# Optimization experiments

Hardware: AMD Instinct MI355X
Metric: run time of the kernel (lower is better)

The kernel has to match this reference:

```python
import jax, jax.numpy as jnp
import numpy as np

D_MODEL = 256
NUM_HEADS = 8
HEAD_DIM = D_MODEL // NUM_HEADS


def setup_inputs() -> dict:
    key = jax.random.key(0)
    ks = jax.random.split(key, 16)
    B, C, H, W = 2, D_MODEL, 64, 64
    s = 0.02
    inp = {
        "query_feat": jax.random.normal(ks[0], (B, C, H, W), jnp.float32),
        "lateral_feat": jax.random.normal(ks[1], (B, C, H, W), jnp.float32),
        # 1x1 convs == per-pixel linear layers: weight (out, in), bias (out,)
        "Wq": jax.random.normal(ks[2], (C, C), jnp.float32) * s,
        "bq": jnp.zeros((C,), jnp.float32),
        "Wk": jax.random.normal(ks[3], (C, C), jnp.float32) * s,
        "bk": jnp.zeros((C,), jnp.float32),
        "Wv": jax.random.normal(ks[4], (C, C), jnp.float32) * s,
        "bv": jnp.zeros((C,), jnp.float32),
        "Wo": jax.random.normal(ks[5], (C, C), jnp.float32) * s,
        "bo": jnp.zeros((C,), jnp.float32),
        "W1": jax.random.normal(ks[6], (4 * C, C), jnp.float32) * s,
        "b1": jnp.zeros((4 * C,), jnp.float32),
        "W2": jax.random.normal(ks[7], (C, 4 * C), jnp.float32) * s,
        "b2": jnp.zeros((C,), jnp.float32),
    }
    return inp


def reference(query_feat, lateral_feat, Wq, bq, Wk, bk, Wv, bv, Wo, bo, W1, b1, W2, b2):
    B, C, H, W = query_feat.shape
    N = H * W
    h, d = NUM_HEADS, HEAD_DIM
    scale = d ** -0.5

    # (B,C,H,W) -> (B,N,C) tokens
    xq = query_feat.reshape(B, C, N).transpose(0, 2, 1)
    xl = lateral_feat.reshape(B, C, N).transpose(0, 2, 1)

    # 1x1-conv projections = dense per-token linear
    Q = (xq @ Wq.T + bq).reshape(B, N, h, d).transpose(0, 2, 1, 3)  # (B,h,N,d)
    K = (xl @ Wk.T + bk).reshape(B, N, h, d).transpose(0, 2, 1, 3)
    V = (xl @ Wv.T + bv).reshape(B, N, h, d).transpose(0, 2, 1, 3)

    scores = jnp.einsum("bhqd,bhkd->bhqk", Q, K) * scale  # (B,h,N,N)
    attn = jax.nn.softmax(scores, axis=-1)  # dropout = identity at inference
    out = jnp.einsum("bhqk,bhkd->bhqd", attn, V)  # (B,h,N,d)

    out = out.transpose(0, 2, 1, 3).reshape(B, N, C)  # (B,N,C)
    out = out @ Wo.T + bo
    out = out.transpose(0, 2, 1).reshape(B, C, H, W)
    out = out + query_feat  # residual

    # MLP on channels (1x1 convs + exact GELU)
    t = out.reshape(B, C, N).transpose(0, 2, 1)  # (B,N,C)
    hdn = jax.nn.gelu(t @ W1.T + b1, approximate=False)  # (B,N,4C)
    mlp = (hdn @ W2.T + b2).transpose(0, 2, 1).reshape(B, C, H, W)
    return out + mlp
```

## Files before the change

kernel.cpp:

```cpp
#include <hip/hip_runtime.h>
#include <math.h>

namespace {

constexpr int kB  = 2;
constexpr int kC  = 256;
constexpr int kN  = 4096;
constexpr int kHD = 32;
constexpr int kC4 = 1024;

typedef __attribute__((ext_vector_type(8))) short bf16x8;
typedef __attribute__((ext_vector_type(4))) float f32x4;
typedef __attribute__((ext_vector_type(16))) float f32x16;

__device__ __forceinline__ float gelu_exact(float x) {
  return 0.5f * x * (1.0f + erff(x * 0.70710678118654752f));
}

__device__ __forceinline__ unsigned short f2bf(float x) {
  unsigned u = __builtin_bit_cast(unsigned, x);
  u += 0x7FFFu + ((u >> 16) & 1u);
  return (unsigned short)(u >> 16);
}

__device__ __forceinline__ float bf2f(unsigned short us) {
  return __builtin_bit_cast(float, (unsigned)us << 16);
}

__device__ __forceinline__ float fast_exp2(float x) {
  int i = (int)__builtin_fmaf(x, 8388608.0f, 1064866805.0f);
  return __builtin_bit_cast(float, i);
}

__device__ __forceinline__ unsigned cvt_pk_bf16(float lo, float hi) {
  unsigned r;
  asm("v_cvt_pk_bf16_f32 %0, %1, %2" : "=v"(r) : "v"(lo), "v"(hi));
  return r;
}

__global__ __launch_bounds__(256)
void convert_all(const float* __restrict__ qfeat, const float* __restrict__ lfeat,
                 const float* __restrict__ Wq, const float* __restrict__ Wk,
                 const float* __restrict__ Wv, const float* __restrict__ Wo,
                 const float* __restrict__ W1, const float* __restrict__ W2,
                 unsigned short* __restrict__ qtok, unsigned short* __restrict__ ltok,
                 unsigned short* __restrict__ wbf)
{
  __shared__ float Lds[32][36];
  const int z = blockIdx.z;
  const int t = threadIdx.x;
  if (z < 4) {
    const float* src = (z < kB) ? qfeat : lfeat;
    unsigned short* dst = (z < kB) ? qtok : ltok;
    const int b = z & 1;
    src += (size_t)b * kC * kN;
    dst += (size_t)b * kN * kC;
    const int n0 = blockIdx.x * 32, c0 = blockIdx.y * 32;
    const int r = t >> 3, q4 = (t & 7) * 4;
    {
      const float4 v = *(const float4*)&src[(size_t)(c0 + r) * kN + n0 + q4];
      Lds[r][q4 + 0] = v.x; Lds[r][q4 + 1] = v.y; Lds[r][q4 + 2] = v.z; Lds[r][q4 + 3] = v.w;
    }
    __syncthreads();
    ushort4 p;
    p.x = f2bf(Lds[q4 + 0][r]); p.y = f2bf(Lds[q4 + 1][r]);
    p.z = f2bf(Lds[q4 + 2][r]); p.w = f2bf(Lds[q4 + 3][r]);
    *(ushort4*)&dst[(size_t)(n0 + r) * kC + c0 + q4] = p;
  } else {
    const int wi = blockIdx.y * 128 + blockIdx.x;
    if (wi >= 768) return;
    const int i4 = wi * 1024 + t * 4;
    const float* s; int base;
    if      (i4 < 65536)  { s = Wq; base = 0; }
    else if (i4 < 131072) { s = Wk; base = 65536; }
    else if (i4 < 196608) { s = Wv; base = 131072; }
    else if (i4 < 262144) { s = Wo; base = 196608; }
    else if (i4 < 524288) { s = W1; base = 262144; }
    else                  { s = W2; base = 524288; }
    const float4 v = *(const float4*)&s[i4 - base];
    ushort4 p;
    p.x = f2bf(v.x); p.y = f2bf(v.y); p.z = f2bf(v.z); p.w = f2bf(v.w);
    *(ushort4*)&wbf[i4] = p;
  }
}

template <int EPI, bool GELU, bool RES>
__global__ __launch_bounds__(256)
void gemm_mfma(const unsigned short* __restrict__ Wbf,
               const unsigned short* __restrict__ Xtok,
               const float* __restrict__ bias, const float* __restrict__ res,
               void* __restrict__ Y1, void* __restrict__ Y2,
               int M, int Nn, int K, float oscale)
{
  __shared__ unsigned short Wlds[64 * 64];
  __shared__ unsigned short Xlds[64 * 64];

  const int z = blockIdx.z;
  Xtok += (size_t)z * Nn * K;

  const int t = threadIdx.x;
  const int w = t >> 6, l = t & 63;
  const int r = l & 15, g = l >> 4;
  const int wm = w >> 1, wn = w & 1;
  const int m0 = blockIdx.y * 64, n0 = blockIdx.x * 64;

  const int rw = t >> 3;
  const int sw = (t & 7) ^ (rw & 7);
  const unsigned short* wsrc = Wbf + (size_t)(m0 + rw) * K + sw * 8;
  const unsigned short* xsrc = Xtok + (size_t)(n0 + rw) * K + sw * 8;

  f32x4 acc[2][2];
#pragma unroll
  for (int i = 0; i < 2; ++i)
#pragma unroll
    for (int j = 0; j < 2; ++j) acc[i][j] = {0.f, 0.f, 0.f, 0.f};

  bf16x8 wrg[2], xrg[2];
#pragma unroll
  for (int j = 0; j < 2; ++j) {
    wrg[j] = *(const bf16x8*)(wsrc + (size_t)(32 * j) * K);
    xrg[j] = *(const bf16x8*)(xsrc + (size_t)(32 * j) * K);
  }

  for (int k0 = 0; k0 < K; k0 += 64) {
    __syncthreads();
    *(bf16x8*)((char*)Wlds + t * 16)         = wrg[0];
    *(bf16x8*)((char*)Wlds + (256 + t) * 16) = wrg[1];
    *(bf16x8*)((char*)Xlds + t * 16)         = xrg[0];
    *(bf16x8*)((char*)Xlds + (256 + t) * 16) = xrg[1];
    __syncthreads();
    if (k0 + 64 < K) {
#pragma unroll
      for (int j = 0; j < 2; ++j) {
        wrg[j] = *(const bf16x8*)(wsrc + (size_t)(32 * j) * K + k0 + 64);
        xrg[j] = *(const bf16x8*)(xsrc + (size_t)(32 * j) * K + k0 + 64);
      }
    }
#pragma unroll
    for (int kc = 0; kc < 2; ++kc) {
      const int sl = ((kc * 4 + g) ^ (r & 7)) * 16;
      bf16x8 a0 = *(const bf16x8*)((const char*)Wlds + (wm * 32 + r) * 128 + sl);
      bf16x8 a1 = *(const bf16x8*)((const char*)Wlds + (wm * 32 + 16 + r) * 128 + sl);
      bf16x8 b0 = *(const bf16x8*)((const char*)Xlds + (wn * 32 + r) * 128 + sl);
      bf16x8 b1 = *(const bf16x8*)((const char*)Xlds + (wn * 32 + 16 + r) * 128 + sl);
      acc[0][0] = __builtin_amdgcn_mfma_f32_16x16x32_bf16(a0, b0, acc[0][0], 0, 0, 0);
      acc[0][1] = __builtin_amdgcn_mfma_f32_16x16x32_bf16(a0, b1, acc[0][1], 0, 0, 0);
      acc[1][0] = __builtin_amdgcn_mfma_f32_16x16x32_bf16(a1, b0, acc[1][0], 0, 0, 0);
      acc[1][1] = __builtin_amdgcn_mfma_f32_16x16x32_bf16(a1, b1, acc[1][1], 0, 0, 0);
    }
  }

#pragma unroll
  for (int f = 0; f < 2; ++f) {
    const int mb = m0 + wm * 32 + f * 16 + 4 * g;
    const float* bp = bias + mb;
    if constexpr (EPI == 4) { if (mb >= (M >> 1)) bp = res + (mb - (M >> 1)); }
    const float4 b4 = *(const float4*)bp;
#pragma unroll
    for (int fn = 0; fn < 2; ++fn) {
      const int n = n0 + wn * 32 + fn * 16 + r;
      float v[4];
      v[0] = (acc[f][fn][0] + b4.x) * oscale; v[1] = (acc[f][fn][1] + b4.y) * oscale;
      v[2] = (acc[f][fn][2] + b4.z) * oscale; v[3] = (acc[f][fn][3] + b4.w) * oscale;
      if (GELU) {
#pragma unroll
        for (int q = 0; q < 4; ++q) v[q] = gelu_exact(v[q]);
      }
      if (RES) {
#pragma unroll
        for (int q = 0; q < 4; ++q)
          v[q] += res[(size_t)z * M * Nn + (size_t)(mb + q) * Nn + n];
      }
      if constexpr (EPI == 1) {
        unsigned short* Yt = (unsigned short*)Y1 + (size_t)z * Nn * M;
        ushort4 pk;
        pk.x = f2bf(v[0]); pk.y = f2bf(v[1]); pk.z = f2bf(v[2]); pk.w = f2bf(v[3]);
        *(ushort4*)&Yt[(size_t)n * M + mb] = pk;
      }
      if constexpr (EPI == 4) {
        const int Mh = M >> 1;
        if (mb < Mh) {
          unsigned short* Yt = (unsigned short*)Y1 + (size_t)z * Nn * Mh;
          ushort4 pk;
          pk.x = f2bf(v[0]); pk.y = f2bf(v[1]); pk.z = f2bf(v[2]); pk.w = f2bf(v[3]);
          *(ushort4*)&Yt[(size_t)n * Mh + mb] = pk;
        } else {
          unsigned short* Yc = (unsigned short*)Y2 + (size_t)z * Mh * Nn;
#pragma unroll
          for (int q = 0; q < 4; ++q) Yc[(size_t)(mb - Mh + q) * Nn + n] = f2bf(v[q]);
        }
      }
      if constexpr (EPI == 6) {
        float* Yf = (float*)Y1 + (size_t)z * M * Nn;
        const unsigned short* Rt = (const unsigned short*)Y2 + (size_t)z * Nn * M;
#pragma unroll
        for (int q = 0; q < 4; ++q)
          Yf[(size_t)(mb + q) * Nn + n] = v[q] + bf2f(Rt[(size_t)n * M + mb + q]);
      }
    }
  }
}

__global__ __launch_bounds__(512, 4)
void attn_mfma32(const unsigned short* __restrict__ Qbf,
                 const unsigned short* __restrict__ Kbf,
                 const unsigned short* __restrict__ Vbf,
                 unsigned short* __restrict__ Aout)
{
  __shared__ __attribute__((aligned(16))) char smem[17408];

  const int id = blockIdx.x;
  const int bh = id & 15;
  const int b = bh >> 3, hd = bh & 7;
  const int t = threadIdx.x;
  const int w = t >> 6, l = t & 63;
  const int r = l & 31, hi = l >> 5;
  const int qg = w >> 1, kh = w & 1;

  const unsigned short* Qb = Qbf + (size_t)b * kN * kC;
  const unsigned short* Kb = Kbf + (size_t)b * kN * kC;
  const unsigned short* Vb = Vbf + ((size_t)b * kC + hd * kHD) * kN;
  unsigned short* Ap = Aout + (size_t)b * kN * kC;

  const int q0 = (id >> 4) * 128 + qg * 32;

  const bf16x8 qf0 = *(const bf16x8*)&Qb[(size_t)(q0 + r) * kC + hd * kHD + hi * 8];
  const bf16x8 qf1 = *(const bf16x8*)&Qb[(size_t)(q0 + r) * kC + hd * kHD + 16 + hi * 8];

  const int tt = t & 255, th = t >> 8;
  const unsigned short* ksrc = Kb + (size_t)(th * 2048 + (tt >> 2)) * kC + hd * kHD + (tt & 3) * 8;
  const unsigned short* vsrc = Vb + (size_t)(tt >> 3) * kN + th * 2048 + (tt & 7) * 8;
  char* kdst = smem + th * 4096 + ((tt & 3) * 64 + ((tt >> 2) ^ (9 * (tt & 3)))) * 16;
  char* vdst = smem + 8192 + th * 4096 + ((tt & 7) * 32 + ((tt >> 3) ^ (tt & 7))) * 16;

  int koff[2][2], voff[2][2];
#pragma unroll
  for (int ds = 0; ds < 2; ++ds)
#pragma unroll
    for (int tile = 0; tile < 2; ++tile) {
      const int c = 2 * ds + hi;
      koff[ds][tile] = kh * 4096 + (c * 64 + tile * 32 + (r ^ (9 * c))) * 16;
    }
#pragma unroll
  for (int ktile = 0; ktile < 2; ++ktile)
#pragma unroll
    for (int kc = 0; kc < 2; ++kc) {
      const int c = ktile * 4 + kc * 2 + hi;
      voff[ktile][kc] = 8192 + kh * 4096 + (c * 32 + (r ^ c)) * 16;
    }

  const f32x16 ZV = {0.f};
  f32x16 oA = ZV, oB = ZV;
  float lsum = 0.f;

  bf16x8 krg = *(const bf16x8*)ksrc;
  bf16x8 vrg = *(const bf16x8*)vsrc;

  for (int kt = 0; kt < 2048; kt += 64) {
    __syncthreads();
    *(bf16x8*)kdst = krg;
    *(bf16x8*)vdst = vrg;
    __syncthreads();
    if (kt + 64 < 2048) {
      krg = *(const bf16x8*)(ksrc + (size_t)(kt + 64) * kC);
      vrg = *(const bf16x8*)(vsrc + kt + 64);
    }

    bf16x8 ka00 = *(const bf16x8*)(smem + koff[0][0]);
    bf16x8 ka10 = *(const bf16x8*)(smem + koff[1][0]);
    bf16x8 ka01 = *(const bf16x8*)(smem + koff[0][1]);
    bf16x8 ka11 = *(const bf16x8*)(smem + koff[1][1]);
    __builtin_amdgcn_s_setprio(1);
    f32x16 s0 = __builtin_amdgcn_mfma_f32_32x32x16_bf16(ka00, qf0, ZV, 0, 0, 0);
    s0        = __builtin_amdgcn_mfma_f32_32x32x16_bf16(ka10, qf1, s0, 0, 0, 0);
    f32x16 s1 = __builtin_amdgcn_mfma_f32_32x32x16_bf16(ka01, qf0, ZV, 0, 0, 0);
    s1        = __builtin_amdgcn_mfma_f32_32x32x16_bf16(ka11, qf1, s1, 0, 0, 0);
    __builtin_amdgcn_s_setprio(0);

#pragma unroll
    for (int ktile = 0; ktile < 2; ++ktile) {
      const f32x16& sv = ktile ? s1 : s0;
      float pe[16];
#pragma unroll
      for (int j = 0; j < 16; ++j) pe[j] = fast_exp2(sv[j]);
      lsum += (((pe[0] + pe[1]) + (pe[2] + pe[3])) + ((pe[4] + pe[5]) + (pe[6] + pe[7])))
            + (((pe[8] + pe[9]) + (pe[10] + pe[11])) + ((pe[12] + pe[13]) + (pe[14] + pe[15])));
      const unsigned c0 = cvt_pk_bf16(pe[0], pe[1]),   c1 = cvt_pk_bf16(pe[2], pe[3]);
      const unsigned c2 = cvt_pk_bf16(pe[4], pe[5]),   c3 = cvt_pk_bf16(pe[6], pe[7]);
      const unsigned c4 = cvt_pk_bf16(pe[8], pe[9]),   c5 = cvt_pk_bf16(pe[10], pe[11]);
      const unsigned c6 = cvt_pk_bf16(pe[12], pe[13]), c7 = cvt_pk_bf16(pe[14], pe[15]);
      auto a02 = __builtin_amdgcn_permlane32_swap(c0, c2, false, false);
      auto a13 = __builtin_amdgcn_permlane32_swap(c1, c3, false, false);
      auto a46 = __builtin_amdgcn_permlane32_swap(c4, c6, false, false);
      auto a57 = __builtin_amdgcn_permlane32_swap(c5, c7, false, false);
      union { unsigned u[4]; bf16x8 v; } p0, p1;
      p0.u[0] = a02[0]; p0.u[1] = a13[0]; p0.u[2] = a02[1]; p0.u[3] = a13[1];
      p1.u[0] = a46[0]; p1.u[1] = a57[0]; p1.u[2] = a46[1]; p1.u[3] = a57[1];
      bf16x8 vf0 = *(const bf16x8*)(smem + voff[ktile][0]);
      bf16x8 vf1 = *(const bf16x8*)(smem + voff[ktile][1]);
      __builtin_amdgcn_s_setprio(1);
      oA = __builtin_amdgcn_mfma_f32_32x32x16_bf16(vf0, p0.v, oA, 0, 0, 0);
      oB = __builtin_amdgcn_mfma_f32_32x32x16_bf16(vf1, p1.v, oB, 0, 0, 0);
      __builtin_amdgcn_s_setprio(0);
    }
  }

  {
    auto pr = __builtin_amdgcn_permlane32_swap(
        __builtin_bit_cast(unsigned, lsum), __builtin_bit_cast(unsigned, lsum), false, false);
    lsum = __builtin_bit_cast(float, (unsigned)pr[0]) + __builtin_bit_cast(float, (unsigned)pr[1]);
  }
  float oS[16];
#pragma unroll
  for (int j = 0; j < 16; ++j) oS[j] = oA[j] + oB[j];

  float* Scr = (float*)smem;
  __syncthreads();
  if (kh == 1) {
    float* S = Scr + ((size_t)qg * 64 + l) * 17;
#pragma unroll
    for (int j = 0; j < 16; ++j) S[j] = oS[j];
    S[16] = lsum;
  }
  __syncthreads();
  if (kh == 0) {
    const float* S = Scr + ((size_t)qg * 64 + l) * 17;
#pragma unroll
    for (int j = 0; j < 16; ++j) oS[j] += S[j];
    lsum += S[16];
    const float inv = 1.f / lsum;

    unsigned* T = (unsigned*)(Scr + (size_t)qg * 64 * 17);
#pragma unroll
    for (int p = 0; p < 8; ++p) {
      const int r2 = 4 * (p >> 1) + 2 * hi + (p & 1);
      T[r2 * 33 + r] = cvt_pk_bf16(oS[2 * p] * inv, oS[2 * p + 1] * inv);
    }
    unsigned v[8];
#pragma unroll
    for (int j = 0; j < 8; ++j) v[j] = T[(8 * hi + j) * 33 + r];
    unsigned short* outp = Ap + (size_t)(q0 + r) * kC + hd * kHD + hi * 16;
    uint4 w0{v[0], v[1], v[2], v[3]}, w1{v[4], v[5], v[6], v[7]};
    *(uint4*)outp = w0;
    *(uint4*)(outp + 8) = w1;
  }
}

}

extern "C" void kernel_launch(void* const* d_in, const int* in_sizes, int n_in,
                              void* d_out, int out_size, void* d_ws, size_t ws_size,
                              hipStream_t stream)
{
  const float* qfeat = (const float*)d_in[0];
  const float* lfeat = (const float*)d_in[1];
  const float* Wq = (const float*)d_in[2];
  const float* bq = (const float*)d_in[3];
  const float* Wk = (const float*)d_in[4];
  const float* bk = (const float*)d_in[5];
  const float* Wv = (const float*)d_in[6];
  const float* bv = (const float*)d_in[7];
  const float* Wo = (const float*)d_in[8];
  const float* bo = (const float*)d_in[9];
  const float* W1 = (const float*)d_in[10];
  const float* b1 = (const float*)d_in[11];
  const float* W2 = (const float*)d_in[12];
  const float* b2 = (const float*)d_in[13];
  float* out = (float*)d_out;
  (void)in_sizes; (void)n_in; (void)out_size; (void)ws_size;

  constexpr float kScaleLog2e = 0.25506970f;

  const size_t bcn = (size_t)kB * kC * kN;
  unsigned short* qtok   = (unsigned short*)d_ws;
  unsigned short* ltok   = qtok + bcn;
  unsigned short* wbf    = ltok + bcn;
  unsigned short* qbf    = wbf + 786432;
  unsigned short* kbf    = qbf + bcn;
  unsigned short* vbf    = kbf + bcn;
  unsigned short* atok   = vbf + bcn;
  unsigned short* owstok = atok + bcn;
  unsigned short* h1tok  = owstok + bcn;

  dim3 blk(256);

  convert_all<<<dim3(128, 8, 5), blk, 0, stream>>>(
      qfeat, lfeat, Wq, Wk, Wv, Wo, W1, W2, qtok, ltok, wbf);

  gemm_mfma<1, false, false><<<dim3(64, 4, 2), blk, 0, stream>>>(
      wbf, qtok, bq, nullptr, qbf, nullptr, kC, kN, kC, kScaleLog2e);
  gemm_mfma<4, false, false><<<dim3(64, 8, 2), blk, 0, stream>>>(
      wbf + 65536, ltok, bk, bv, kbf, vbf, 2 * kC, kN, kC, 1.0f);

  attn_mfma32<<<dim3(512), dim3(512), 0, stream>>>(qbf, kbf, vbf, atok);

  gemm_mfma<1, false, true><<<dim3(64, 4, 2), blk, 0, stream>>>(
      wbf + 196608, atok, bo, qfeat, owstok, nullptr, kC, kN, kC, 1.0f);
  gemm_mfma<1, true, false><<<dim3(64, 16, 2), blk, 0, stream>>>(
      wbf + 262144, owstok, b1, nullptr, h1tok, nullptr, kC4, kN, kC, 1.0f);
  gemm_mfma<6, false, false><<<dim3(64, 4, 2), blk, 0, stream>>>(
      wbf + 524288, h1tok, b2, nullptr, out, owstok, kC, kN, kC4, 1.0f);
}
```

Measured before the change: 108.2 us.

## Double-buffer K/V LDS tiles and use hardware exp2 in attention

The attention loop now alternates between two LDS buffers, so each iteration needs one barrier instead of two: the next tile is stored into the other buffer while the current one is consumed. The software bit-trick exp2 approximation is replaced with the hardware v_exp_f32 instruction, which is more accurate and may use fewer VALU ops. LDS use per block grows to 32KB, which could reduce occupancy at 4 blocks per CU.

```diff
diff --git a/kernel.cpp b/kernel.cpp
--- a/kernel.cpp
+++ b/kernel.cpp
@@ -27,9 +27,14 @@
   return __builtin_bit_cast(float, (unsigned)us << 16);
 }
 
-__device__ __forceinline__ float fast_exp2(float x) {
-  int i = (int)__builtin_fmaf(x, 8388608.0f, 1064866805.0f);
-  return __builtin_bit_cast(float, i);
+__device__ __forceinline__ float exp2_hw(float x) {
+#if __has_builtin(__builtin_amdgcn_exp2f)
+  return __builtin_amdgcn_exp2f(x);
+#else
+  float r;
+  asm("v_exp_f32 %0, %1\n\ts_nop 1" : "=v"(r) : "v"(x));
+  return r;
+#endif
 }
 
 __device__ __forceinline__ unsigned cvt_pk_bf16(float lo, float hi) {
@@ -207,7 +212,7 @@
                  const unsigned short* __restrict__ Vbf,
                  unsigned short* __restrict__ Aout)
 {
-  __shared__ __attribute__((aligned(16))) char smem[17408];
+  __shared__ __attribute__((aligned(16))) char smem[32768];
 
   const int id = blockIdx.x;
   const int bh = id & 15;
@@ -256,20 +261,20 @@
   bf16x8 krg = *(const bf16x8*)ksrc;
   bf16x8 vrg = *(const bf16x8*)vsrc;
 
-  for (int kt = 0; kt < 2048; kt += 64) {
+  for (int it = 0; it < 32; ++it) {
+    const int bo = (it & 1) << 14;
+    *(bf16x8*)(kdst + bo) = krg;
+    *(bf16x8*)(vdst + bo) = vrg;
+    if (it + 1 < 32) {
+      krg = *(const bf16x8*)(ksrc + (size_t)(it + 1) * 64 * kC);
+      vrg = *(const bf16x8*)(vsrc + (it + 1) * 64);
+    }
     __syncthreads();
-    *(bf16x8*)kdst = krg;
-    *(bf16x8*)vdst = vrg;
-    __syncthreads();
-    if (kt + 64 < 2048) {
-      krg = *(const bf16x8*)(ksrc + (size_t)(kt + 64) * kC);
-      vrg = *(const bf16x8*)(vsrc + kt + 64);
-    }
-
-    bf16x8 ka00 = *(const bf16x8*)(smem + koff[0][0]);
-    bf16x8 ka10 = *(const bf16x8*)(smem + koff[1][0]);
-    bf16x8 ka01 = *(const bf16x8*)(smem + koff[0][1]);
-    bf16x8 ka11 = *(const bf16x8*)(smem + koff[1][1]);
+
+    bf16x8 ka00 = *(const bf16x8*)(smem + bo + koff[0][0]);
+    bf16x8 ka10 = *(const bf16x8*)(smem + bo + koff[1][0]);
+    bf16x8 ka01 = *(const bf16x8*)(smem + bo + koff[0][1]);
+    bf16x8 ka11 = *(const bf16x8*)(smem + bo + koff[1][1]);
     __builtin_amdgcn_s_setprio(1);
     f32x16 s0 = __builtin_amdgcn_mfma_f32_32x32x16_bf16(ka00, qf0, ZV, 0, 0, 0);
     s0        = __builtin_amdgcn_mfma_f32_32x32x16_bf16(ka10, qf1, s0, 0, 0, 0);
@@ -282,7 +287,7 @@
       const f32x16& sv = ktile ? s1 : s0;
       float pe[16];
 #pragma unroll
-      for (int j = 0; j < 16; ++j) pe[j] = fast_exp2(sv[j]);
+      for (int j = 0; j < 16; ++j) pe[j] = exp2_hw(sv[j]);
       lsum += (((pe[0] + pe[1]) + (pe[2] + pe[3])) + ((pe[4] + pe[5]) + (pe[6] + pe[7])))
             + (((pe[8] + pe[9]) + (pe[10] + pe[11])) + ((pe[12] + pe[13]) + (pe[14] + pe[15])));
       const unsigned c0 = cvt_pk_bf16(pe[0], pe[1]),   c1 = cvt_pk_bf16(pe[2], pe[3]);
@@ -296,8 +301,8 @@
       union { unsigned u[4]; bf16x8 v; } p0, p1;
       p0.u[0] = a02[0]; p0.u[1] = a13[0]; p0.u[2] = a02[1]; p0.u[3] = a13[1];
       p1.u[0] = a46[0]; p1.u[1] = a57[0]; p1.u[2] = a46[1]; p1.u[3] = a57[1];
-      bf16x8 vf0 = *(const bf16x8*)(smem + voff[ktile][0]);
-      bf16x8 vf1 = *(const bf16x8*)(smem + voff[ktile][1]);
+      bf16x8 vf0 = *(const bf16x8*)(smem + bo + voff[ktile][0]);
+      bf16x8 vf1 = *(const bf16x8*)(smem + bo + voff[ktile][1]);
       __builtin_amdgcn_s_setprio(1);
       oA = __builtin_amdgcn_mfma_f32_32x32x16_bf16(vf0, p0.v, oA, 0, 0, 0);
       oB = __builtin_amdgcn_mfma_f32_32x32x16_bf16(vf1, p1.v, oB, 0, 0, 0);
```

Measured after the change: 103.7 us. 4.2% less time.
